# Kernel optimization log

Hardware: AMD Instinct MI355X
Metric: run time of the kernel (lower is better)

Reference implementation:

```python
import jax, jax.numpy as jnp
import numpy as np

NUM_EDGES_POOL = 10000
OUT_DIM = 64
IN_DIM = 128
E_SEL = 50000


def setup_inputs() -> dict:
    key = jax.random.key(0)
    k1, k2, k3 = jax.random.split(key, 3)
    nodes_features_input = jax.random.normal(k1, (E_SEL, IN_DIM, 1), dtype=jnp.float32)
    edges_index = jax.random.randint(k2, (E_SEL,), 0, NUM_EDGES_POOL, dtype=jnp.int32)
    # glorot_normal over (out, in) fan dims
    std = np.sqrt(2.0 / (OUT_DIM + IN_DIM)).astype(np.float32)
    edges_input_core = jax.random.normal(k3, (NUM_EDGES_POOL, OUT_DIM, IN_DIM), dtype=jnp.float32) * std
    edges_input_bias = jnp.zeros((NUM_EDGES_POOL, OUT_DIM, 1), dtype=jnp.float32)
    return {
        "nodes_features_input": nodes_features_input,
        "edges_index": edges_index,
        "edges_input_core": edges_input_core,
        "edges_input_bias": edges_input_bias,
    }


def reference(nodes_features_input, edges_index, edges_input_core, edges_input_bias):
    # Gather per-edge weight and bias from the shared pool
    W = edges_input_core[edges_index]          # [E, out, in]
    b = edges_input_bias[edges_index]          # [E, out, 1]
    # Batched matmul: [E, out, in] @ [E, in, 1] -> [E, out, 1]
    y = jnp.einsum('eoi,eik->eok', W, nodes_features_input) + b
    return jax.nn.relu(y)
```

## Files before the change

kernel.cpp:

```cpp
#include <hip/hip_runtime.h>

#define IN_DIM 128
#define OUT_DIM 64
#define MAXCHUNK 64


__global__ void init_head_kernel(int* __restrict__ head, int P) {
    int i = blockIdx.x * 256 + threadIdx.x;
    if (i < P) head[i] = -1;
}

__global__ void build_lists_kernel(const int* __restrict__ idx,
                                   int* __restrict__ head,
                                   int* __restrict__ nextp, int E) {
    int e = blockIdx.x * 256 + threadIdx.x;
    if (e < E) {
        int p = idx[e];
        int old = atomicExch(&head[p], e);
        nextp[e] = old;
    }
}

__global__ __launch_bounds__(256) void gemv_pool_kernel(
    const float* __restrict__ x,
    const float* __restrict__ Wpool,
    const float* __restrict__ bpool,
    float*       __restrict__ out,
    const int*   __restrict__ head,
    const int*   __restrict__ nextp)
{
    __shared__ float4 Ws[32][OUT_DIM + 1];
    __shared__ float  bs[OUT_DIM];
    __shared__ float  xs[4][IN_DIM];
    __shared__ int    elist[MAXCHUNK];
    __shared__ int    ecount;
    __shared__ int    ecur;

    const int p = blockIdx.x;
    const int h = head[p];
    if (h < 0) return;

    const int wave = threadIdx.x >> 6;
    const int lane = threadIdx.x & 63;

    if (wave == 0) {
        bs[lane] = bpool[(size_t)p * OUT_DIM + lane];
        if (lane == 0) {
            int n = 0, c = h;
            while (c >= 0 && n < MAXCHUNK) { elist[n++] = c; c = nextp[c]; }
            ecount = n;
            ecur = c;
        }
    } else {
        const float4* Wg = reinterpret_cast<const float4*>(
            Wpool + (size_t)p * (OUT_DIM * IN_DIM));
        for (int q = threadIdx.x - 64; q < OUT_DIM * 32; q += 192) {
            int o = q >> 5, i4 = q & 31;
            Ws[i4][o] = Wg[q];
        }
    }
    __syncthreads();

    while (true) {
        const int n = ecount;
        for (int j = wave; j < n; j += 4) {
            const int e = elist[j];
            const float2 xv = reinterpret_cast<const float2*>(
                x + (size_t)e * IN_DIM)[lane];
            reinterpret_cast<float2*>(xs[wave])[lane] = xv;
            const float4* xrow = reinterpret_cast<const float4*>(xs[wave]);
            float ax = 0.f, ay = 0.f, az = 0.f, aw = 0.f;
            #pragma unroll 8
            for (int i4 = 0; i4 < 32; ++i4) {
                const float4 w  = Ws[i4][lane];
                const float4 xq = xrow[i4];
                ax += w.x * xq.x;
                ay += w.y * xq.y;
                az += w.z * xq.z;
                aw += w.w * xq.w;
            }
            const float acc = (ax + ay) + (az + aw) + bs[lane];
            out[(size_t)e * OUT_DIM + lane] = fmaxf(acc, 0.f);
        }
        if (n < MAXCHUNK) break;
        __syncthreads();
        if (threadIdx.x == 0) {
            int nn = 0, c = ecur;
            while (c >= 0 && nn < MAXCHUNK) { elist[nn++] = c; c = nextp[c]; }
            ecount = nn;
            ecur = c;
        }
        __syncthreads();
    }
}

extern "C" void kernel_launch(void* const* d_in, const int* in_sizes, int n_in,
                              void* d_out, int out_size, void* d_ws, size_t ws_size,
                              hipStream_t stream) {
    const float* x    = (const float*)d_in[0];
    const int*   idx  = (const int*)d_in[1];
    const float* W    = (const float*)d_in[2];
    const float* b    = (const float*)d_in[3];
    float* out = (float*)d_out;

    const int E = in_sizes[1];
    const int P = in_sizes[2] / (OUT_DIM * IN_DIM);

    int* head  = (int*)d_ws;
    int* nextp = head + P;

    init_head_kernel<<<(P + 255) / 256, 256, 0, stream>>>(head, P);
    build_lists_kernel<<<(E + 255) / 256, 256, 0, stream>>>(idx, head, nextp, E);
    gemv_pool_kernel<<<P, 256, 0, stream>>>(x, W, b, out, head, nextp);
}
```

Measured before the change: 469.3 us.

## Replace linked-list edge grouping with CSR buckets and async LDS weight loads

```diff
diff --git a/kernel.cpp b/kernel.cpp
--- a/kernel.cpp
+++ b/kernel.cpp
@@ -2,22 +2,58 @@
 
 #define IN_DIM 128
 #define OUT_DIM 64
-#define MAXCHUNK 64
+
+typedef __attribute__((address_space(1))) const void gvoid_t;
+typedef __attribute__((address_space(3))) void lvoid_t;
 
 
-__global__ void init_head_kernel(int* __restrict__ head, int P) {
+__global__ void zero_counts_kernel(int* __restrict__ counts, int P) {
     int i = blockIdx.x * 256 + threadIdx.x;
-    if (i < P) head[i] = -1;
+    if (i < P) counts[i] = 0;
 }
 
-__global__ void build_lists_kernel(const int* __restrict__ idx,
-                                   int* __restrict__ head,
-                                   int* __restrict__ nextp, int E) {
+__global__ void count_kernel(const int* __restrict__ idx,
+                             int* __restrict__ counts, int E) {
+    int e = blockIdx.x * 256 + threadIdx.x;
+    if (e < E) atomicAdd(&counts[idx[e]], 1);
+}
+
+__global__ __launch_bounds__(1024) void scan_kernel(
+    const int* __restrict__ counts, int* __restrict__ offs,
+    int* __restrict__ cursor, int P) {
+    __shared__ int part[1024];
+    const int t = threadIdx.x;
+    const int chunk = (P + 1023) >> 10;
+    const int lo = t * chunk;
+    const int hi = (lo + chunk < P) ? (lo + chunk) : P;
+    int s = 0;
+    for (int i = lo; i < hi; ++i) s += counts[i];
+    part[t] = s;
+    __syncthreads();
+    for (int d = 1; d < 1024; d <<= 1) {
+        int v = (t >= d) ? part[t - d] : 0;
+        __syncthreads();
+        part[t] += v;
+        __syncthreads();
+    }
+    int base = (t == 0) ? 0 : part[t - 1];
+    for (int i = lo; i < hi; ++i) {
+        offs[i] = base;
+        cursor[i] = 0;
+        base += counts[i];
+    }
+    if (t == 1023) offs[P] = part[1023];
+}
+
+__global__ void scatter_kernel(const int* __restrict__ idx,
+                               const int* __restrict__ offs,
+                               int* __restrict__ cursor,
+                               int* __restrict__ edge_ids, int E) {
     int e = blockIdx.x * 256 + threadIdx.x;
     if (e < E) {
         int p = idx[e];
-        int old = atomicExch(&head[p], e);
-        nextp[e] = old;
+        int pos = atomicAdd(&cursor[p], 1);
+        edge_ids[offs[p] + pos] = e;
     }
 }
 
@@ -26,71 +62,68 @@
     const float* __restrict__ Wpool,
     const float* __restrict__ bpool,
     float*       __restrict__ out,
-    const int*   __restrict__ head,
-    const int*   __restrict__ nextp)
+    const int*   __restrict__ offs,
+    const int*   __restrict__ edge_ids)
 {
-    __shared__ float4 Ws[32][OUT_DIM + 1];
-    __shared__ float  bs[OUT_DIM];
-    __shared__ float  xs[4][IN_DIM];
-    __shared__ int    elist[MAXCHUNK];
-    __shared__ int    ecount;
-    __shared__ int    ecur;
+    __shared__ float Wlds[OUT_DIM * IN_DIM];
+    __shared__ float xs[4][IN_DIM];
 
     const int p = blockIdx.x;
-    const int h = head[p];
-    if (h < 0) return;
+    const int start = offs[p];
+    const int n = offs[p + 1] - start;
+    if (n == 0) return;
 
     const int wave = threadIdx.x >> 6;
     const int lane = threadIdx.x & 63;
 
-    if (wave == 0) {
-        bs[lane] = bpool[(size_t)p * OUT_DIM + lane];
-        if (lane == 0) {
-            int n = 0, c = h;
-            while (c >= 0 && n < MAXCHUNK) { elist[n++] = c; c = nextp[c]; }
-            ecount = n;
-            ecur = c;
-        }
-    } else {
-        const float4* Wg = reinterpret_cast<const float4*>(
-            Wpool + (size_t)p * (OUT_DIM * IN_DIM));
-        for (int q = threadIdx.x - 64; q < OUT_DIM * 32; q += 192) {
-            int o = q >> 5, i4 = q & 31;
-            Ws[i4][o] = Wg[q];
-        }
+    const float* Wp = Wpool + (size_t)p * (OUT_DIM * IN_DIM);
+    #pragma unroll
+    for (int j = 0; j < 8; ++j) {
+        const int s  = ((wave << 3) + j) * 64 + lane;
+        const int o  = s >> 5;
+        const int i4 = s & 31;
+        const float* g = Wp + o * IN_DIM + ((i4 ^ (o & 7)) << 2);
+        lvoid_t* ldst = (lvoid_t*)((char*)Wlds + (size_t)((wave << 3) + j) * 1024);
+        __builtin_amdgcn_global_load_lds((gvoid_t*)g, ldst, 16, 0, 0);
+    }
+
+    const float bv = bpool[(size_t)p * OUT_DIM + lane];
+
+    const int j0 = wave;
+    int e0 = -1;
+    if (j0 < n) {
+        e0 = edge_ids[start + j0];
+        const float2 xv = reinterpret_cast<const float2*>(
+            x + (size_t)e0 * IN_DIM)[lane];
+        reinterpret_cast<float2*>(xs[wave])[lane] = xv;
     }
     __syncthreads();
 
-    while (true) {
-        const int n = ecount;
-        for (int j = wave; j < n; j += 4) {
-            const int e = elist[j];
+    for (int j = j0; j < n; j += 4) {
+        int e;
+        if (j == j0) {
+            e = e0;
+        } else {
+            e = edge_ids[start + j];
             const float2 xv = reinterpret_cast<const float2*>(
                 x + (size_t)e * IN_DIM)[lane];
             reinterpret_cast<float2*>(xs[wave])[lane] = xv;
-            const float4* xrow = reinterpret_cast<const float4*>(xs[wave]);
-            float ax = 0.f, ay = 0.f, az = 0.f, aw = 0.f;
-            #pragma unroll 8
-            for (int i4 = 0; i4 < 32; ++i4) {
-                const float4 w  = Ws[i4][lane];
-                const float4 xq = xrow[i4];
-                ax += w.x * xq.x;
-                ay += w.y * xq.y;
-                az += w.z * xq.z;
-                aw += w.w * xq.w;
-            }
-            const float acc = (ax + ay) + (az + aw) + bs[lane];
-            out[(size_t)e * OUT_DIM + lane] = fmaxf(acc, 0.f);
         }
-        if (n < MAXCHUNK) break;
-        __syncthreads();
-        if (threadIdx.x == 0) {
-            int nn = 0, c = ecur;
-            while (c >= 0 && nn < MAXCHUNK) { elist[nn++] = c; c = nextp[c]; }
-            ecount = nn;
-            ecur = c;
+        const float4* xrow = reinterpret_cast<const float4*>(xs[wave]);
+        float ax = 0.f, ay = 0.f, az = 0.f, aw = 0.f;
+        #pragma unroll
+        for (int i4 = 0; i4 < 32; ++i4) {
+            const float4 w = *reinterpret_cast<const float4*>(
+                reinterpret_cast<const char*>(Wlds)
+                + (lane << 9) + ((i4 ^ (lane & 7)) << 4));
+            const float4 xq = xrow[i4];
+            ax += w.x * xq.x;
+            ay += w.y * xq.y;
+            az += w.z * xq.z;
+            aw += w.w * xq.w;
         }
-        __syncthreads();
+        const float acc = (ax + ay) + (az + aw) + bv;
+        out[(size_t)e * OUT_DIM + lane] = fmaxf(acc, 0.f);
     }
 }
 
@@ -106,10 +139,14 @@
     const int E = in_sizes[1];
     const int P = in_sizes[2] / (OUT_DIM * IN_DIM);
 
-    int* head  = (int*)d_ws;
-    int* nextp = head + P;
+    int* counts   = (int*)d_ws;
+    int* offs     = counts + P;
+    int* cursor   = offs + P + 1;
+    int* edge_ids = cursor + P;
 
-    init_head_kernel<<<(P + 255) / 256, 256, 0, stream>>>(head, P);
-    build_lists_kernel<<<(E + 255) / 256, 256, 0, stream>>>(idx, head, nextp, E);
-    gemv_pool_kernel<<<P, 256, 0, stream>>>(x, W, b, out, head, nextp);
+    zero_counts_kernel<<<(P + 255) / 256, 256, 0, stream>>>(counts, P);
+    count_kernel<<<(E + 255) / 256, 256, 0, stream>>>(idx, counts, E);
+    scan_kernel<<<1, 1024, 0, stream>>>(counts, offs, cursor, P);
+    scatter_kernel<<<(E + 255) / 256, 256, 0, stream>>>(idx, offs, cursor, edge_ids, E);
+    gemv_pool_kernel<<<P, 256, 0, stream>>>(x, W, b, out, offs, edge_ids);
 }
```

Measured after the change: 480.4 us. +2.4%, slower.

## Load weight tile via direct global-to-LDS with XOR swizzle and prefetch next x row

Applied to the files above, without the earlier changes.

```diff
diff --git a/kernel.cpp b/kernel.cpp
--- a/kernel.cpp
+++ b/kernel.cpp
@@ -4,11 +4,8 @@
 #define OUT_DIM 64
 #define MAXCHUNK 64
 
-
-__global__ void init_head_kernel(int* __restrict__ head, int P) {
-    int i = blockIdx.x * 256 + threadIdx.x;
-    if (i < P) head[i] = -1;
-}
+typedef __attribute__((address_space(1))) const void gvoid_t;
+typedef __attribute__((address_space(3))) void lvoid_t;
 
 __global__ void build_lists_kernel(const int* __restrict__ idx,
                                    int* __restrict__ head,
@@ -16,8 +13,7 @@
     int e = blockIdx.x * 256 + threadIdx.x;
     if (e < E) {
         int p = idx[e];
-        int old = atomicExch(&head[p], e);
-        nextp[e] = old;
+        nextp[e] = atomicExch(&head[p], e);
     }
 }
 
@@ -29,12 +25,11 @@
     const int*   __restrict__ head,
     const int*   __restrict__ nextp)
 {
-    __shared__ float4 Ws[32][OUT_DIM + 1];
-    __shared__ float  bs[OUT_DIM];
-    __shared__ float  xs[4][IN_DIM];
-    __shared__ int    elist[MAXCHUNK];
-    __shared__ int    ecount;
-    __shared__ int    ecur;
+    __shared__ float Wlds[OUT_DIM * IN_DIM];
+    __shared__ float xs[4][IN_DIM];
+    __shared__ int   elist[MAXCHUNK];
+    __shared__ int   ecount;
+    __shared__ int   ecur;
 
     const int p = blockIdx.x;
     const int h = head[p];
@@ -43,45 +38,59 @@
     const int wave = threadIdx.x >> 6;
     const int lane = threadIdx.x & 63;
 
-    if (wave == 0) {
-        bs[lane] = bpool[(size_t)p * OUT_DIM + lane];
-        if (lane == 0) {
-            int n = 0, c = h;
-            while (c >= 0 && n < MAXCHUNK) { elist[n++] = c; c = nextp[c]; }
-            ecount = n;
-            ecur = c;
-        }
-    } else {
-        const float4* Wg = reinterpret_cast<const float4*>(
-            Wpool + (size_t)p * (OUT_DIM * IN_DIM));
-        for (int q = threadIdx.x - 64; q < OUT_DIM * 32; q += 192) {
-            int o = q >> 5, i4 = q & 31;
-            Ws[i4][o] = Wg[q];
-        }
+    const float* Wp = Wpool + (size_t)p * (OUT_DIM * IN_DIM);
+    #pragma unroll
+    for (int j = 0; j < 8; ++j) {
+        const int s  = ((wave << 3) + j) * 64 + lane;
+        const int o  = s >> 5;
+        const int i4 = s & 31;
+        const float* g = Wp + o * IN_DIM + ((i4 ^ (o & 7)) << 2);
+        lvoid_t* ldst = (lvoid_t*)((char*)Wlds + (size_t)((wave << 3) + j) * 1024);
+        __builtin_amdgcn_global_load_lds((gvoid_t*)g, ldst, 16, 0, 0);
+    }
+
+    const float bv = bpool[(size_t)p * OUT_DIM + lane];
+
+    if (threadIdx.x == 0) {
+        int nn = 0, c = h;
+        while (c >= 0 && nn < MAXCHUNK) { elist[nn++] = c; c = nextp[c]; }
+        ecount = nn;
+        ecur = c;
     }
     __syncthreads();
 
     while (true) {
         const int n = ecount;
+        int e = (wave < n) ? elist[wave] : -1;
+        float2 xr = make_float2(0.f, 0.f);
+        if (e >= 0)
+            xr = reinterpret_cast<const float2*>(x + (size_t)e * IN_DIM)[lane];
+
         for (int j = wave; j < n; j += 4) {
-            const int e = elist[j];
-            const float2 xv = reinterpret_cast<const float2*>(
-                x + (size_t)e * IN_DIM)[lane];
-            reinterpret_cast<float2*>(xs[wave])[lane] = xv;
+            reinterpret_cast<float2*>(xs[wave])[lane] = xr;
+            const int en = (j + 4 < n) ? elist[j + 4] : -1;
+            float2 xn = make_float2(0.f, 0.f);
+            if (en >= 0)
+                xn = reinterpret_cast<const float2*>(x + (size_t)en * IN_DIM)[lane];
+
             const float4* xrow = reinterpret_cast<const float4*>(xs[wave]);
             float ax = 0.f, ay = 0.f, az = 0.f, aw = 0.f;
-            #pragma unroll 8
+            #pragma unroll
             for (int i4 = 0; i4 < 32; ++i4) {
-                const float4 w  = Ws[i4][lane];
+                const float4 w = *reinterpret_cast<const float4*>(
+                    reinterpret_cast<const char*>(Wlds)
+                    + (lane << 9) + ((i4 ^ (lane & 7)) << 4));
                 const float4 xq = xrow[i4];
                 ax += w.x * xq.x;
                 ay += w.y * xq.y;
                 az += w.z * xq.z;
                 aw += w.w * xq.w;
             }
-            const float acc = (ax + ay) + (az + aw) + bs[lane];
-            out[(size_t)e * OUT_DIM + lane] = fmaxf(acc, 0.f);
+            out[(size_t)e * OUT_DIM + lane] = fmaxf((ax + ay) + (az + aw) + bv, 0.f);
+            e = en;
+            xr = xn;
         }
+
         if (n < MAXCHUNK) break;
         __syncthreads();
         if (threadIdx.x == 0) {
@@ -109,7 +118,7 @@
     int* head  = (int*)d_ws;
     int* nextp = head + P;
 
-    init_head_kernel<<<(P + 255) / 256, 256, 0, stream>>>(head, P);
+    hipMemsetAsync(head, 0xFF, (size_t)P * sizeof(int), stream);
     build_lists_kernel<<<(E + 255) / 256, 256, 0, stream>>>(idx, head, nextp, E);
     gemv_pool_kernel<<<P, 256, 0, stream>>>(x, W, b, out, head, nextp);
 }
```

Measured after the change: 461.0 us. About the same (-1.8%).
